# Performance work log

Measured on AMD Instinct MI355X. Metric: run time of the kernel, lower is better.

Reference implementation:

```python
import jax, jax.numpy as jnp
import numpy as np
from jax import lax

EPS_BN = 1e-5
SMOOTH = 1e-5


def conv3x3(x, w):
    # x: [N,C,H,W], w: [O,I,3,3], stride 1, padding 1 (SAME)
    return lax.conv_general_dilated(
        x, w, window_strides=(1, 1), padding='SAME',
        dimension_numbers=('NCHW', 'OIHW', 'NCHW'))


def batchnorm(x, gamma, beta):
    # training-mode BatchNorm2d: batch statistics over (N,H,W), biased var
    mean = jnp.mean(x, axis=(0, 2, 3), keepdims=True)
    var = jnp.mean(jnp.square(x - mean), axis=(0, 2, 3), keepdims=True)
    g = gamma.reshape(1, -1, 1, 1)
    b = beta.reshape(1, -1, 1, 1)
    return (x - mean) * lax.rsqrt(var + EPS_BN) * g + b


def tanimoto(a, b, axes):
    tpl = jnp.sum(a * b, axis=axes, keepdims=True)
    sq = jnp.sum(a * a + b * b, axis=axes, keepdims=True)
    return (tpl + SMOOTH) / (sq - tpl + SMOOTH)


def tanimoto_compl(a, b, axes):
    return 0.5 * (tanimoto(a, b, axes) + tanimoto(1.0 - a, 1.0 - b, axes))


def setup_inputs() -> dict:
    key = jax.random.key(0)
    ks = jax.random.split(key, 5)
    N, Cin, Cout, H, W = 8, 64, 64, 256, 256
    x = jax.random.normal(ks[0], (N, Cin, H, W), dtype=jnp.float32)
    fan = Cin * 9
    wq = jax.random.normal(ks[1], (Cout, Cin, 3, 3), dtype=jnp.float32) / np.sqrt(fan)
    wk = jax.random.normal(ks[2], (Cout, Cin, 3, 3), dtype=jnp.float32) / np.sqrt(fan)
    wv = jax.random.normal(ks[3], (Cout, Cin, 3, 3), dtype=jnp.float32) / np.sqrt(fan)
    ones = jnp.ones((Cout,), dtype=jnp.float32)
    zeros = jnp.zeros((Cout,), dtype=jnp.float32)
    return {
        'x': x,
        'wq': wq, 'gq': ones, 'bq': zeros,
        'wk': wk, 'gk': ones, 'bk': zeros,
        'wv': wv, 'gv': ones, 'bv': zeros,
        'g_norm': ones, 'b_norm': zeros,
    }


def reference(x, wq, gq, bq, wk, gk, bk, wv, gv, bv, g_norm, b_norm):
    q = jax.nn.sigmoid(batchnorm(conv3x3(x, wq), gq, bq))
    k = jax.nn.sigmoid(batchnorm(conv3x3(x, wk), gk, bk))
    v = jax.nn.sigmoid(batchnorm(conv3x3(x, wv), gv, bv))
    attn_spatial = tanimoto_compl(q, k, axes=(1,))      # [N,1,H,W]
    attn_channel = tanimoto_compl(q, k, axes=(2, 3))    # [N,C,1,1]
    attention = 0.5 * (attn_spatial * v + attn_channel * v)
    return batchnorm(attention, g_norm, b_norm)
```

## Files before the change

### kernel.cpp

```cpp
#include <hip/hip_runtime.h>

typedef unsigned short u16;
typedef __attribute__((ext_vector_type(8))) short short8;
typedef __attribute__((ext_vector_type(4))) float f32x4;

#define OFF_SUMS 0ul
#define OFF_WT   26624ul
#define OFF_ASP  247808ul
#define OFF_CONV 2344960ul
#define S_SUM   0
#define S_SSQ   768
#define S_SC    1536
#define S_BI    1728
#define M_A1    1920
#define M_A23   2432
#define M_A45   2944
#define M_V1    3456
#define M_V2    3968
#define M_AV    4480
#define M_AV2   4992
#define M_A2V2  5504
#define S_ACH   6016
#define S_SCA   6528
#define S_BIA   6592
#define S_NFLOAT 6656

__device__ __forceinline__ float bf2f(u16 v) {
  union { unsigned u; float f; } x; x.u = ((unsigned)v) << 16; return x.f;
}
__device__ __forceinline__ u16 f2bf(float f) {
  union { float f; unsigned u; } x; x.f = f;
  unsigned r = x.u + 0x7fffu + ((x.u >> 16) & 1u);
  return (u16)(r >> 16);
}
__device__ __forceinline__ float sigmoidf_(float x) { return 1.f / (1.f + __expf(-x)); }

__global__ void transpose_k(const float* __restrict__ x, u16* __restrict__ xt) {
  __shared__ u16 t[64][130];
  const int bid = blockIdx.x;
  const int wtile = bid & 1, h = (bid >> 1) & 255, n = bid >> 9;
  const int w0 = wtile << 7;
  const int tid = threadIdx.x;
  for (int i = tid; i < 8192; i += 256) {
    int c = i >> 7, w = i & 127;
    t[c][w] = f2bf(x[(((n << 6) + c) << 16) + (h << 8) + w0 + w]);
  }
  __syncthreads();
  for (int i = tid; i < 8192; i += 256) {
    int w = i >> 6, c = i & 63;
    xt[(long)((((n << 8) + h) << 8) + w0 + w) * 64 + c] = t[c][w];
  }
}

__global__ void repack_k(const float* __restrict__ wq, const float* __restrict__ wk,
                         const float* __restrict__ wv, u16* __restrict__ wt) {
  int i = blockIdx.x * 256 + threadIdx.x;
  if (i >= 110592) return;
  int conv = i / 36864, j = i % 36864;
  int oc = j / 576, r2 = j % 576, c = r2 / 9, dd = r2 % 9;
  const float* src = conv == 0 ? wq : (conv == 1 ? wk : wv);
  wt[(dd * 192 + conv * 64 + oc) * 64 + c] = f2bf(src[j]);
}

__global__ __launch_bounds__(256, 2) void conv_k(const u16* __restrict__ xt,
                                                 const u16* __restrict__ wt,
                                                 u16* __restrict__ conv,
                                                 float* __restrict__ S) {
  __shared__ u16 lx[3 * 130 * 72];
  const int bid = blockIdx.x;
  const int wtile = bid & 1, h = (bid >> 1) & 255, n = bid >> 9;
  const int w0 = wtile << 7;
  const int tid = threadIdx.x;
  for (int g = tid; g < 3120; g += 256) {
    int row = g / 1040;
    int r2 = g - row * 1040;
    int w = r2 >> 3, cg = r2 & 7;
    int hs = h + row - 1, wsr = w0 + w - 1;
    uint4 val = make_uint4(0u, 0u, 0u, 0u);
    if ((unsigned)hs < 256u && (unsigned)wsr < 256u)
      val = *(const uint4*)(xt + (long)((((n << 8) + hs) << 8) + wsr) * 64 + (cg << 3));
    *(uint4*)(&lx[row * 9360 + w * 72 + (cg << 3)]) = val;
  }
  __syncthreads();
  const int lane = tid & 63, wave = tid >> 6;
  const int quad = lane >> 4, l15 = lane & 15;
  f32x4 acc[3][8];
#pragma unroll
  for (int a = 0; a < 3; ++a)
#pragma unroll
    for (int b = 0; b < 8; ++b) acc[a][b] = (f32x4){0.f, 0.f, 0.f, 0.f};

#pragma unroll
  for (int dy = 0; dy < 3; ++dy) {
#pragma unroll
    for (int dx = 0; dx < 3; ++dx) {
      const u16* wp = wt + (dy * 3 + dx) * 12288;
      short8 bfr[3][2];
#pragma unroll
      for (int nt = 0; nt < 3; ++nt)
#pragma unroll
        for (int kc = 0; kc < 2; ++kc)
          bfr[nt][kc] = *(const short8*)(wp + ((wave * 3 + nt) * 16 + l15) * 64 + kc * 32 + quad * 8);
#pragma unroll
      for (int kc = 0; kc < 2; ++kc) {
        short8 afr[8];
#pragma unroll
        for (int mt = 0; mt < 8; ++mt)
          afr[mt] = *(const short8*)(&lx[dy * 9360 + (mt * 16 + l15 + dx) * 72 + kc * 32 + quad * 8]);
#pragma unroll
        for (int mt = 0; mt < 8; ++mt)
#pragma unroll
          for (int nt = 0; nt < 3; ++nt)
            acc[nt][mt] = __builtin_amdgcn_mfma_f32_16x16x32_bf16(afr[mt], bfr[nt][kc], acc[nt][mt], 0, 0, 0);
      }
    }
  }
  const long pix0 = (long)bid * 128;
#pragma unroll
  for (int nt = 0; nt < 3; ++nt) {
    const int oc = (wave * 3 + nt) * 16 + l15;
#pragma unroll
    for (int mt = 0; mt < 8; ++mt) {
      const long pr = pix0 + mt * 16 + quad * 4;
#pragma unroll
      for (int r = 0; r < 4; ++r)
        conv[(pr + r) * 192 + oc] = f2bf(acc[nt][mt][r]);
    }
  }
  const int sh = (bid & 3) * 192;
#pragma unroll
  for (int nt = 0; nt < 3; ++nt) {
    float s = 0.f, ss = 0.f;
#pragma unroll
    for (int mt = 0; mt < 8; ++mt)
#pragma unroll
      for (int r = 0; r < 4; ++r) {
        float x = acc[nt][mt][r];
        s += x; ss += x * x;
      }
    s += __shfl_xor(s, 16); ss += __shfl_xor(ss, 16);
    s += __shfl_xor(s, 32); ss += __shfl_xor(ss, 32);
    if (lane < 16) {
      const int oc = (wave * 3 + nt) * 16 + l15;
      atomicAdd(&S[S_SUM + sh + oc], s);
      atomicAdd(&S[S_SSQ + sh + oc], ss);
    }
  }
}

__global__ void bnparam_k(float* __restrict__ S, const float* gq, const float* bq, const float* gk,
                          const float* bk, const float* gv, const float* bv) {
  int t = threadIdx.x;
  int cv = t >> 6, c = t & 63;
  float g = cv == 0 ? gq[c] : (cv == 1 ? gk[c] : gv[c]);
  float b = cv == 0 ? bq[c] : (cv == 1 ? bk[c] : bv[c]);
  float sm = 0.f, sq = 0.f;
#pragma unroll
  for (int sh = 0; sh < 4; ++sh) { sm += S[S_SUM + sh * 192 + t]; sq += S[S_SSQ + sh * 192 + t]; }
  const float inv = 1.f / 524288.f;
  float mean = sm * inv;
  float var = sq * inv - mean * mean;
  float rstd = rsqrtf(var + 1e-5f);
  float sc = g * rstd;
  S[S_SC + t] = sc;
  S[S_BI + t] = b - mean * sc;
}

__global__ void k3_k(const u16* __restrict__ conv, float* __restrict__ S, float* __restrict__ asp) {
  __shared__ float red[4][8][64];
  const int tid = threadIdx.x, lane = tid & 63, wave = tid >> 6;
  const int bid = blockIdx.x;
  const int n = bid >> 9;
  const long p0 = (long)bid * 128 + wave * 32;
  const float sq = S[S_SC + lane], bq = S[S_BI + lane];
  const float sk = S[S_SC + 64 + lane], bk = S[S_BI + 64 + lane];
  const float sv = S[S_SC + 128 + lane], bv = S[S_BI + 128 + lane];
  float A1 = 0.f, A23 = 0.f, A45 = 0.f, V1 = 0.f, V2 = 0.f, AV = 0.f, AV2 = 0.f, A2V2 = 0.f;
  float myasp = 0.f;
#pragma unroll 4
  for (int i = 0; i < 32; ++i) {
    const u16* row = conv + (p0 + i) * 192;
    float q = sigmoidf_(bf2f(row[lane]) * sq + bq);
    float k = sigmoidf_(bf2f(row[64 + lane]) * sk + bk);
    float v = sigmoidf_(bf2f(row[128 + lane]) * sv + bv);
    float s1 = q * k, s23 = q * q + k * k, s45 = q + k;
    A1 += s1; A23 += s23; A45 += s45;
#pragma unroll
    for (int m = 1; m < 64; m <<= 1) {
      s1 += __shfl_xor(s1, m);
      s23 += __shfl_xor(s23, m);
      s45 += __shfl_xor(s45, m);
    }
    const float sm = 1e-5f;
    float t1 = (s1 + sm) / (s23 - s1 + sm);
    float t2 = (64.f - s45 + s1 + sm) / (64.f - s45 + s23 - s1 + sm);
    float a = 0.5f * (t1 + t2);
    if (i == (lane & 31)) myasp = a;
    float av = a * v;
    V1 += v; V2 += v * v; AV += av; AV2 += av * v; A2V2 += av * av;
  }
  if (lane < 32) asp[p0 + lane] = myasp;
  red[wave][0][lane] = A1;  red[wave][1][lane] = A23; red[wave][2][lane] = A45;
  red[wave][3][lane] = V1;  red[wave][4][lane] = V2;  red[wave][5][lane] = AV;
  red[wave][6][lane] = AV2; red[wave][7][lane] = A2V2;
  __syncthreads();
  if (tid < 64) {
    const int mb[8] = {M_A1, M_A23, M_A45, M_V1, M_V2, M_AV, M_AV2, M_A2V2};
#pragma unroll
    for (int m = 0; m < 8; ++m) {
      float t = red[0][m][tid] + red[1][m][tid] + red[2][m][tid] + red[3][m][tid];
      atomicAdd(&S[mb[m] + n * 64 + tid], t);
    }
  }
}

__global__ void k4_k(float* __restrict__ S, const float* gn, const float* bn_) {
  __shared__ float r1[512], r2[512];
  const int t = threadIdx.x;
  float A1 = S[M_A1 + t], A23 = S[M_A23 + t], A45 = S[M_A45 + t];
  const float sm = 1e-5f, cnt = 65536.f;
  float t1 = (A1 + sm) / (A23 - A1 + sm);
  float t2 = (cnt - A45 + A1 + sm) / (cnt - A45 + A23 - A1 + sm);
  float ach = 0.5f * (t1 + t2);
  S[S_ACH + t] = ach;
  r1[t] = 0.5f * (S[M_AV + t] + ach * S[M_V1 + t]);
  r2[t] = 0.25f * (S[M_A2V2 + t] + 2.f * ach * S[M_AV2 + t] + ach * ach * S[M_V2 + t]);
  __syncthreads();
  if (t < 64) {
    float s = 0.f, ss = 0.f;
#pragma unroll
    for (int n = 0; n < 8; ++n) { s += r1[n * 64 + t]; ss += r2[n * 64 + t]; }
    const float inv = 1.f / 524288.f;
    float mean = s * inv;
    float var = ss * inv - mean * mean;
    float rstd = rsqrtf(var + 1e-5f);
    float sc = gn[t] * rstd;
    S[S_SCA + t] = sc;
    S[S_BIA + t] = bn_[t] - mean * sc;
  }
}

__global__ void k6_k(const u16* __restrict__ conv, const float* __restrict__ S,
                     const float* __restrict__ asp, float* __restrict__ out) {
  __shared__ float t[128][65];
  const int tid = threadIdx.x, lane = tid & 63, wave = tid >> 6;
  const int n = blockIdx.x >> 9;
  const int hw0 = (blockIdx.x & 511) << 7;
  const long P0 = (long)blockIdx.x * 128;
  const float sv = S[S_SC + 128 + lane], bv = S[S_BI + 128 + lane];
  const float av = S[S_ACH + n * 64 + lane];
  const float sA = S[S_SCA + lane], bA = S[S_BIA + lane];
  for (int i = wave; i < 128; i += 4) {
    const long p = P0 + i;
    float v = sigmoidf_(bf2f(conv[p * 192 + 128 + lane]) * sv + bv);
    float att = 0.5f * (asp[p] + av) * v;
    t[i][lane] = att * sA + bA;
  }
  __syncthreads();
  const int c = tid >> 2, sub = tid & 3;
  const long plane = ((long)((n << 6) + c)) << 16;
  for (int i = 0; i < 8; ++i) {
    const int pst = (i * 4 + sub) << 2;
    f32x4 vbuf;
#pragma unroll
    for (int j = 0; j < 4; ++j) vbuf[j] = t[pst + j][c];
    *(f32x4*)(&out[plane + hw0 + pst]) = vbuf;
  }
}

extern "C" void kernel_launch(void* const* d_in, const int* in_sizes, int n_in,
                              void* d_out, int out_size, void* d_ws, size_t ws_size,
                              hipStream_t stream) {
  (void)in_sizes; (void)n_in; (void)out_size; (void)ws_size;
  const float* x  = (const float*)d_in[0];
  const float* wq = (const float*)d_in[1];
  const float* gq = (const float*)d_in[2];
  const float* bq = (const float*)d_in[3];
  const float* wk = (const float*)d_in[4];
  const float* gk = (const float*)d_in[5];
  const float* bk = (const float*)d_in[6];
  const float* wv = (const float*)d_in[7];
  const float* gv = (const float*)d_in[8];
  const float* bv = (const float*)d_in[9];
  const float* gn = (const float*)d_in[10];
  const float* bn_ = (const float*)d_in[11];
  char* ws = (char*)d_ws;
  float* S   = (float*)(ws + OFF_SUMS);
  u16* wt    = (u16*)(ws + OFF_WT);
  float* asp = (float*)(ws + OFF_ASP);
  u16* conv  = (u16*)(ws + OFF_CONV);
  float* out = (float*)d_out;
  u16* xt  = (u16*)d_out;

  hipMemsetAsync(S, 0, S_NFLOAT * 4, stream);
  transpose_k<<<4096, 256, 0, stream>>>(x, xt);
  repack_k<<<432, 256, 0, stream>>>(wq, wk, wv, wt);
  conv_k<<<4096, 256, 0, stream>>>(xt, wt, conv, S);
  bnparam_k<<<1, 192, 0, stream>>>(S, gq, bq, gk, bk, gv, bv);
  k3_k<<<4096, 256, 0, stream>>>(conv, S, asp);
  k4_k<<<1, 512, 0, stream>>>(S, gn, bn_);
  k6_k<<<4096, 256, 0, stream>>>(conv, S, asp, out);
}
```

Measured before the change: 608.7 us.

## Retile conv into 2x64 pixel blocks with swizzled LDS and higher occupancy

Each conv block now covers two output rows by 64 columns instead of one row by 128, so the staged input halo shrinks from 3x130 to 4x66 pixels and LDS per block drops sharply. The unpadded LDS rows use an XOR swizzle to avoid bank conflicts, and launch bounds go from 2 to 4 blocks per SM. The aim is more resident waves for latency hiding and a smaller halo overhead. Requesting 4 blocks per SM may force register spilling given the 96-float accumulator array.

```diff
diff --git a/kernel.cpp b/kernel.cpp
--- a/kernel.cpp
+++ b/kernel.cpp
@@ -62,24 +62,25 @@
   wt[(dd * 192 + conv * 64 + oc) * 64 + c] = f2bf(src[j]);
 }
 
-__global__ __launch_bounds__(256, 2) void conv_k(const u16* __restrict__ xt,
+__global__ __launch_bounds__(256, 4) void conv_k(const u16* __restrict__ xt,
                                                  const u16* __restrict__ wt,
                                                  u16* __restrict__ conv,
                                                  float* __restrict__ S) {
-  __shared__ u16 lx[3 * 130 * 72];
+  __shared__ u16 lx[4 * 4224];
   const int bid = blockIdx.x;
-  const int wtile = bid & 1, h = (bid >> 1) & 255, n = bid >> 9;
-  const int w0 = wtile << 7;
+  const int wb = bid & 3, hb = (bid >> 2) & 127, n = bid >> 9;
+  const int w0 = wb << 6;
   const int tid = threadIdx.x;
-  for (int g = tid; g < 3120; g += 256) {
-    int row = g / 1040;
-    int r2 = g - row * 1040;
-    int w = r2 >> 3, cg = r2 & 7;
-    int hs = h + row - 1, wsr = w0 + w - 1;
+  for (int g = tid; g < 2112; g += 256) {
+    int row = g / 528;
+    int r2 = g - row * 528;
+    int px = r2 >> 3, cg = r2 & 7;
+    int hs = (hb << 1) + row - 1, wsr = w0 + px - 1;
     uint4 val = make_uint4(0u, 0u, 0u, 0u);
     if ((unsigned)hs < 256u && (unsigned)wsr < 256u)
       val = *(const uint4*)(xt + (long)((((n << 8) + hs) << 8) + wsr) * 64 + (cg << 3));
-    *(uint4*)(&lx[row * 9360 + w * 72 + (cg << 3)]) = val;
+    int idx = ((px << 6) + (cg << 3)) ^ ((px & 7) << 3);
+    *(uint4*)(&lx[row * 4224 + idx]) = val;
   }
   __syncthreads();
   const int lane = tid & 63, wave = tid >> 6;
@@ -105,8 +106,12 @@
       for (int kc = 0; kc < 2; ++kc) {
         short8 afr[8];
 #pragma unroll
-        for (int mt = 0; mt < 8; ++mt)
-          afr[mt] = *(const short8*)(&lx[dy * 9360 + (mt * 16 + l15 + dx) * 72 + kc * 32 + quad * 8]);
+        for (int mt = 0; mt < 8; ++mt) {
+          const int r = mt >> 2;
+          const int wloc = ((mt & 3) << 4) + l15 + dx;
+          int idx = ((wloc << 6) + (kc << 5) + (quad << 3)) ^ ((wloc & 7) << 3);
+          afr[mt] = *(const short8*)(&lx[(r + dy) * 4224 + idx]);
+        }
 #pragma unroll
         for (int mt = 0; mt < 8; ++mt)
 #pragma unroll
@@ -115,16 +120,19 @@
       }
     }
   }
-  const long pix0 = (long)bid * 128;
+  const long prow0 = (long)(((n << 8) + (hb << 1)) << 8) + w0;
 #pragma unroll
   for (int nt = 0; nt < 3; ++nt) {
     const int oc = (wave * 3 + nt) * 16 + l15;
 #pragma unroll
     for (int mt = 0; mt < 8; ++mt) {
-      const long pr = pix0 + mt * 16 + quad * 4;
-#pragma unroll
-      for (int r = 0; r < 4; ++r)
-        conv[(pr + r) * 192 + oc] = f2bf(acc[nt][mt][r]);
+      const int l0 = mt * 16 + quad * 4;
+#pragma unroll
+      for (int r = 0; r < 4; ++r) {
+        const int l = l0 + r;
+        const long pix = prow0 + ((l >> 6) << 8) + (l & 63);
+        conv[pix * 192 + oc] = f2bf(acc[nt][mt][r]);
+      }
     }
   }
   const int sh = (bid & 3) * 192;
```

Measured after the change: 1.568 ms. 158% more time.
